# Performance work log

Measured on AMD Instinct MI355X. Metric: run time of the kernel, lower is better.

Reference implementation:

```python
import jax, jax.numpy as jnp
import numpy as np

B, T, D, NH, V, L = 2, 1024, 1024, 16, 32000, 4  # L = blocks * layers_per_block
HD = D // NH
FF = 4 * D


def rmsnorm(x, gamma, beta):
    # matches RMSNorm: mean of squares over last dim (tp pmean is identity on 1 device)
    ms = jnp.mean(jnp.square(x), axis=-1, keepdims=True)
    return (x / jnp.sqrt(ms + 1e-6)) * gamma + beta


def setup_inputs() -> dict:
    key = jax.random.key(0)
    ks = jax.random.split(key, 16)
    s = 0.02
    inp = {
        "tokens": jax.random.randint(ks[0], (B, T), 0, V, dtype=jnp.int32),
        "emb_W": jax.random.normal(ks[1], (V, D), jnp.float32) * s,
        "pos_W": jax.random.normal(ks[2], (T, D), jnp.float32) * s,
        "g1": jnp.ones((L, D), jnp.float32),
        "be1": jnp.zeros((L, D), jnp.float32),
        "Wqkv": jax.random.normal(ks[3], (L, D, 3 * D), jnp.float32) * s,
        "bqkv": jnp.zeros((L, 3 * D), jnp.float32),
        "Wo": jax.random.normal(ks[4], (L, D, D), jnp.float32) * s,
        "bo": jnp.zeros((L, D), jnp.float32),
        "g2": jnp.ones((L, D), jnp.float32),
        "be2": jnp.zeros((L, D), jnp.float32),
        "Wf1": jax.random.normal(ks[5], (L, D, FF), jnp.float32) * s,
        "bf1": jnp.zeros((L, FF), jnp.float32),
        "Wf2": jax.random.normal(ks[6], (L, FF, D), jnp.float32) * s,
        "bf2": jnp.zeros((L, D), jnp.float32),
        "gf": jnp.ones((D,), jnp.float32),
        "bef": jnp.zeros((D,), jnp.float32),
    }
    return inp


def _forward(tokens, emb_W, pos_W, g1, be1, Wqkv, bqkv, Wo, bo, g2, be2,
             Wf1, bf1, Wf2, bf2, gf, bef):
    x = emb_W[tokens] + pos_W[jnp.arange(T)]  # [B, T, D]
    causal = jnp.tril(jnp.ones((T, T), dtype=bool))
    scale = HD ** -0.5
    for i in range(L):
        # attention sub-block
        h = rmsnorm(x, g1[i], be1[i])
        qkv = h @ Wqkv[i] + bqkv[i]
        q, k, v = jnp.split(qkv, 3, axis=-1)
        q = q.reshape(B, T, NH, HD).transpose(0, 2, 1, 3)  # B nh T d
        k = k.reshape(B, T, NH, HD).transpose(0, 2, 1, 3)
        v = v.reshape(B, T, NH, HD).transpose(0, 2, 1, 3)
        att = jnp.einsum('bhqd,bhkd->bhqk', q, k) * scale
        att = jnp.where(causal, att, -jnp.inf)
        att = jax.nn.softmax(att, axis=-1)
        o = jnp.einsum('bhqk,bhkd->bhqd', att, v)
        o = o.transpose(0, 2, 1, 3).reshape(B, T, D)
        x = x + (o @ Wo[i] + bo[i])
        # FFN sub-block (selu, dropout off since train=False)
        h = rmsnorm(x, g2[i], be2[i])
        f = jax.nn.selu(h @ Wf1[i] + bf1[i]) @ Wf2[i] + bf2[i]
        x = x + f
    # tied output head: final RMSNorm then embedding.attend
    x = rmsnorm(x, gf, bef)
    logits = jnp.einsum('btd,vd->btv', x, emb_W)
    return logits


def reference(tokens, emb_W, pos_W, g1, be1, Wqkv, bqkv, Wo, bo, g2, be2,
              Wf1, bf1, Wf2, bf2, gf, bef):
    return _forward(tokens, emb_W, pos_W, g1, be1, Wqkv, bqkv, Wo, bo,
                    g2, be2, Wf1, bf1, Wf2, bf2, gf, bef)
```

## Files before the change

### kernel.cpp

```cpp
#include <hip/hip_runtime.h>

typedef unsigned short u16;
typedef __attribute__((ext_vector_type(8))) short bf16x8;
typedef __attribute__((ext_vector_type(4))) float f32x4;

#define DD 1024
#define TT 1024
#define NHH 16
#define VV 32000
#define FFF 4096
#define LL 4
#define MM 2048
#define TD3 3072

__device__ __forceinline__ u16 f2bfu(float f) {
  unsigned int x = __builtin_bit_cast(unsigned int, f);
  return (u16)((x + 0x7FFFu + ((x >> 16) & 1u)) >> 16);
}

__device__ __forceinline__ void gl16(const u16* g, u16* l) {
  __builtin_amdgcn_global_load_lds((const __attribute__((address_space(1))) void*)g,
                                   (__attribute__((address_space(3))) void*)l, 16, 0, 0);
}

template <int N>
__device__ __forceinline__ void vwait() {
  if constexpr (N == 0) asm volatile("s_waitcnt vmcnt(0)" ::: "memory");
  else asm volatile("s_waitcnt vmcnt(8)" ::: "memory");
}

__global__ void transpose_cvt_k(const float* __restrict__ in, u16* __restrict__ out,
                                int K, int N) {
  const size_t mat = (size_t)K * N;
  in += (size_t)blockIdx.z * mat;
  out += (size_t)blockIdx.z * mat;
  __shared__ float tile[32][33];
  const int n0 = blockIdx.x << 5, k0 = blockIdx.y << 5;
  const int tx = threadIdx.x, ty = threadIdx.y;
#pragma unroll
  for (int i = 0; i < 32; i += 8) tile[ty + i][tx] = in[(size_t)(k0 + ty + i) * N + n0 + tx];
  __syncthreads();
#pragma unroll
  for (int i = 0; i < 32; i += 8)
    out[(size_t)(n0 + ty + i) * K + k0 + tx] = f2bfu(tile[tx][ty + i]);
}

__global__ void cvt_bf16_k(const float* __restrict__ in, u16* __restrict__ out, long n4) {
  const long i = (long)blockIdx.x * blockDim.x + threadIdx.x;
  if (i >= n4) return;
  const float4 v = ((const float4*)in)[i];
  ushort4 o;
  o.x = f2bfu(v.x); o.y = f2bfu(v.y); o.z = f2bfu(v.z); o.w = f2bfu(v.w);
  ((ushort4*)out)[i] = o;
}

__global__ void embed_k(const int* __restrict__ tok, const float* __restrict__ emb,
                        const float* __restrict__ pos, float* __restrict__ x) {
  const int m = blockIdx.x, tid = threadIdx.x;
  const int t = m & (TT - 1);
  const int id = tok[m];
  const float4 e = ((const float4*)(emb + (size_t)id * DD))[tid];
  const float4 p = ((const float4*)(pos + (size_t)t * DD))[tid];
  float4 r;
  r.x = e.x + p.x; r.y = e.y + p.y; r.z = e.z + p.z; r.w = e.w + p.w;
  ((float4*)(x + (size_t)m * DD))[tid] = r;
}

__global__ void rmsnorm_k(const float* __restrict__ x, const float* __restrict__ g,
                          const float* __restrict__ be, u16* __restrict__ out) {
  const int row = blockIdx.x, tid = threadIdx.x;
  const float4 xv = ((const float4*)(x + (size_t)row * DD))[tid];
  float ss = xv.x * xv.x + xv.y * xv.y + xv.z * xv.z + xv.w * xv.w;
#pragma unroll
  for (int o = 32; o; o >>= 1) ss += __shfl_xor(ss, o);
  __shared__ float sm[4];
  if ((tid & 63) == 0) sm[tid >> 6] = ss;
  __syncthreads();
  const float tot = sm[0] + sm[1] + sm[2] + sm[3];
  const float rs = rsqrtf(tot * (1.f / DD) + 1e-6f);
  const float4 gv = ((const float4*)g)[tid];
  const float4 bv = ((const float4*)be)[tid];
  ushort4 o4;
  o4.x = f2bfu(xv.x * rs * gv.x + bv.x);
  o4.y = f2bfu(xv.y * rs * gv.y + bv.y);
  o4.z = f2bfu(xv.z * rs * gv.z + bv.z);
  o4.w = f2bfu(xv.w * rs * gv.w + bv.w);
  ((ushort4*)(out + (size_t)row * DD))[tid] = o4;
}

template <int NP>
__global__ void addres_k(float* __restrict__ x, const float* __restrict__ pp,
                         const float* __restrict__ bias) {
  const int i = blockIdx.x * 256 + threadIdx.x;
  const int col4 = i & (DD / 4 - 1);
  const float4 bv = ((const float4*)bias)[col4];
  float4 s = ((float4*)x)[i];
  s.x += bv.x; s.y += bv.y; s.z += bv.z; s.w += bv.w;
#pragma unroll
  for (int p = 0; p < NP; ++p) {
    const float4 pv = ((const float4*)pp)[(size_t)p * (MM * DD / 4) + i];
    s.x += pv.x; s.y += pv.y; s.z += pv.z; s.w += pv.w;
  }
  ((float4*)x)[i] = s;
}

__global__ void pack_vt_k(const u16* __restrict__ qkv, u16* __restrict__ Vt) {
  const int z = blockIdx.x;
  const int t0 = blockIdx.y << 6;
  const int b = z >> 4, h = z & 15;
  __shared__ u16 tile[64][72];
  const int tid = threadIdx.x;
  for (int c = tid; c < 512; c += 256) {
    const int t = c >> 3, d8 = (c & 7) << 3;
    union { uint4 u; u16 s[8]; } tmp;
    tmp.u = *(const uint4*)(qkv + (long)(b * TT + t0 + t) * TD3 + 2 * DD + h * 64 + d8);
#pragma unroll
    for (int j = 0; j < 8; ++j) tile[d8 + j][t] = tmp.s[j];
  }
  __syncthreads();
  for (int c = tid; c < 512; c += 256) {
    const int d = c >> 3, t8 = (c & 7) << 3;
    *(uint4*)(Vt + ((long)z * 64 + d) * TT + t0 + t8) = *(const uint4*)&tile[d][t8];
  }
}

__global__ __launch_bounds__(256) void flash_k(const u16* __restrict__ qkv,
                                               const u16* __restrict__ Vt,
                                               u16* __restrict__ o) {
  const int z = blockIdx.x;
  const int pair = blockIdx.y;
  const int b = z >> 4, h = z & 15;
  const int tid = threadIdx.x;
  const int lane = tid & 63;
  const int w = tid >> 6;

  __shared__ u16 Qs[64 * 64];
  __shared__ u16 Ks[128 * 64];
  __shared__ u16 Vs[64 * 128];
  __shared__ u16 Ps[64 * 128];

  const u16* qbase = qkv + (size_t)b * TT * TD3;
  const int kcb = (lane >> 4) << 4;

  for (int half = 0; half < 2; ++half) {
    const int qa = half ? (15 - pair) : pair;
    const int q0 = qa << 6;
    const int nkt = (qa >> 1) + 1;

#pragma unroll
    for (int c = 0; c < 2; ++c) {
      const int rbase = c * 32 + w * 8;
      const int row = rbase + (lane >> 3);
      const u16* src = qbase + (long)(q0 + row) * TD3 + h * 64 +
                       ((((lane & 7) << 4) ^ ((row & 7) << 4)) >> 1);
      gl16(src, &Qs[rbase * 64]);
    }

    float m_r[4], l_r[4];
    f32x4 oacc[4];
#pragma unroll
    for (int r = 0; r < 4; ++r) { m_r[r] = -1e30f; l_r[r] = 0.f; }
#pragma unroll
    for (int nd = 0; nd < 4; ++nd) oacc[nd] = (f32x4){0.f, 0.f, 0.f, 0.f};

    for (int kt = 0; kt < nkt; ++kt) {
      const int t0 = kt << 7;
#pragma unroll
      for (int c = 0; c < 4; ++c) {
        const int rbase = c * 32 + w * 8;
        const int row = rbase + (lane >> 3);
        const u16* src = qbase + (long)(t0 + row) * TD3 + DD + h * 64 +
                         ((((lane & 7) << 4) ^ ((row & 7) << 4)) >> 1);
        gl16(src, &Ks[rbase * 64]);
      }
#pragma unroll
      for (int c = 0; c < 4; ++c) {
        const int rbase = c * 16 + w * 4;
        const int d = rbase + (lane >> 4);
        const u16* src = Vt + ((long)(z * 64 + d)) * TT + t0 +
                         ((((lane & 15) << 4) ^ ((d & 7) << 4)) >> 1);
        gl16(src, &Vs[rbase * 128]);
      }
      __syncthreads();

      f32x4 sacc[8];
#pragma unroll
      for (int ni = 0; ni < 8; ++ni) sacc[ni] = (f32x4){0.f, 0.f, 0.f, 0.f};
      const int qrow = (w << 4) + (lane & 15);
#pragma unroll
      for (int ks = 0; ks < 2; ++ks) {
        const bf16x8 aq = *(const bf16x8*)&Qs[qrow * 64 + (((ks * 64 + kcb) ^ ((qrow & 7) << 4)) >> 1)];
#pragma unroll
        for (int ni = 0; ni < 8; ++ni) {
          const int key = (lane & 15) + (ni << 4);
          const bf16x8 bk = *(const bf16x8*)&Ks[key * 64 + (((ks * 64 + kcb) ^ ((key & 7) << 4)) >> 1)];
          sacc[ni] = __builtin_amdgcn_mfma_f32_16x16x32_bf16(aq, bk, sacc[ni], 0, 0, 0);
        }
      }

      float mx[4] = {-1e30f, -1e30f, -1e30f, -1e30f};
      const bool diag = (kt == nkt - 1);
#pragma unroll
      for (int ni = 0; ni < 8; ++ni)
#pragma unroll
        for (int r = 0; r < 4; ++r) {
          float v = sacc[ni][r] * 0.125f;
          if (diag) {
            const int key = t0 + (lane & 15) + (ni << 4);
            const int qq = q0 + (w << 4) + ((lane >> 4) << 2) + r;
            if (key > qq) v = -1e30f;
          }
          sacc[ni][r] = v;
          mx[r] = fmaxf(mx[r], v);
        }
#pragma unroll
      for (int st = 1; st < 16; st <<= 1)
#pragma unroll
        for (int r = 0; r < 4; ++r) mx[r] = fmaxf(mx[r], __shfl_xor(mx[r], st));
      float sc[4], sum[4];
#pragma unroll
      for (int r = 0; r < 4; ++r) {
        const float mn = fmaxf(m_r[r], mx[r]);
        sc[r] = __expf(m_r[r] - mn);
        m_r[r] = mn;
        sum[r] = 0.f;
      }
#pragma unroll
      for (int ni = 0; ni < 8; ++ni)
#pragma unroll
        for (int r = 0; r < 4; ++r) {
          const float e = __expf(sacc[ni][r] - m_r[r]);
          sum[r] += e;
          const int prow = (w << 4) + ((lane >> 4) << 2) + r;
          const int pcol = (lane & 15) + (ni << 4);
          Ps[prow * 128 + (((pcol << 1) ^ ((prow & 7) << 4)) >> 1)] = f2bfu(e);
        }
#pragma unroll
      for (int st = 1; st < 16; st <<= 1)
#pragma unroll
        for (int r = 0; r < 4; ++r) sum[r] += __shfl_xor(sum[r], st);
#pragma unroll
      for (int r = 0; r < 4; ++r) l_r[r] = l_r[r] * sc[r] + sum[r];
#pragma unroll
      for (int nd = 0; nd < 4; ++nd)
#pragma unroll
        for (int r = 0; r < 4; ++r) oacc[nd][r] *= sc[r];

#pragma unroll
      for (int ks2 = 0; ks2 < 4; ++ks2) {
        const int prow = (w << 4) + (lane & 15);
        const bf16x8 pa = *(const bf16x8*)&Ps[prow * 128 + (((ks2 * 64 + kcb) ^ ((prow & 7) << 4)) >> 1)];
#pragma unroll
        for (int nd = 0; nd < 4; ++nd) {
          const int dd2 = (lane & 15) + (nd << 4);
          const bf16x8 vb = *(const bf16x8*)&Vs[dd2 * 128 + (((ks2 * 64 + kcb) ^ ((dd2 & 7) << 4)) >> 1)];
          oacc[nd] = __builtin_amdgcn_mfma_f32_16x16x32_bf16(pa, vb, oacc[nd], 0, 0, 0);
        }
      }
      __syncthreads();
    }

    float inv[4];
#pragma unroll
    for (int r = 0; r < 4; ++r) inv[r] = 1.f / l_r[r];
#pragma unroll
    for (int nd = 0; nd < 4; ++nd)
#pragma unroll
      for (int r = 0; r < 4; ++r) {
        const int row = q0 + (w << 4) + ((lane >> 4) << 2) + r;
        const int col = (h << 6) + (lane & 15) + (nd << 4);
        o[(long)(b * TT + row) * DD + col] = f2bfu(oacc[nd][r] * inv[r]);
      }
  }
}

enum { EPI_BF16 = 0, EPI_BF16_BIAS = 1, EPI_SELU = 2, EPI_F32 = 3, EPI_RESID = 4 };

template <int EPI>
__global__ __launch_bounds__(256) void gemm_bt(
    const u16* __restrict__ A, long az1, long az2, int lda,
    const u16* __restrict__ Bt, long bz1, long bz2, int ldb,
    void* __restrict__ C, long cz1, long cz2, int ldc,
    const float* __restrict__ bias, int Nvalid, int K) {
  const int z = blockIdx.z;
  A += (long)(z >> 4) * az1 + (long)(z & 15) * az2;
  Bt += (long)(z >> 4) * bz1 + (long)(z & 15) * bz2;
  const long coff = (long)(z >> 4) * cz1 + (long)(z & 15) * cz2;

  __shared__ u16 ldsA[2][128 * 32];
  __shared__ u16 ldsB[2][128 * 32];

  const int tid = threadIdx.x;
  const int lane = tid & 63;
  const int wave = tid >> 6;
  const int wr = wave >> 1, wc = wave & 1;
  const int m0 = blockIdx.x << 7, n0 = blockIdx.y << 7;

  f32x4 acc[4][4];
#pragma unroll
  for (int i = 0; i < 4; ++i)
#pragma unroll
    for (int j = 0; j < 4; ++j) acc[i][j] = (f32x4){0.f, 0.f, 0.f, 0.f};

  auto STAGE = [&](int buf, int kt) {
    const int k0 = kt << 5;
#pragma unroll
    for (int p = 0; p < 2; ++p) {
      const int c = tid + (p << 8);
      const int row = c >> 2, col = (c & 3) << 3;
      gl16(A + (long)(m0 + row) * lda + k0 + col, &ldsA[buf][c << 3]);
      gl16(Bt + (long)(n0 + row) * ldb + k0 + col, &ldsB[buf][c << 3]);
    }
  };

  const int nk = K >> 5;
  STAGE(0, 0);
  __syncthreads();
  int cur = 0;
  for (int kt = 0; kt < nk; ++kt) {
    if (kt + 1 < nk) STAGE(cur ^ 1, kt + 1);
    const int rb = lane & 15;
    const int kc = (lane >> 4) << 3;
    bf16x8 af[4], bfr[4];
#pragma unroll
    for (int mi = 0; mi < 4; ++mi)
      af[mi] = *(const bf16x8*)&ldsA[cur][(((wr << 6) + (mi << 4) + rb) << 5) + kc];
#pragma unroll
    for (int ni = 0; ni < 4; ++ni)
      bfr[ni] = *(const bf16x8*)&ldsB[cur][(((wc << 6) + (ni << 4) + rb) << 5) + kc];
#pragma unroll
    for (int mi = 0; mi < 4; ++mi)
#pragma unroll
      for (int ni = 0; ni < 4; ++ni)
        acc[mi][ni] = __builtin_amdgcn_mfma_f32_16x16x32_bf16(af[mi], bfr[ni], acc[mi][ni], 0, 0, 0);
    __syncthreads();
    cur ^= 1;
  }

  const int row0 = m0 + (wr << 6) + ((lane >> 4) << 2);
  const int col0 = n0 + (wc << 6) + (lane & 15);
#pragma unroll
  for (int ni = 0; ni < 4; ++ni) {
    const int col = col0 + (ni << 4);
    if (col >= Nvalid) continue;
    float bv = 0.f;
    if (EPI == EPI_BF16_BIAS || EPI == EPI_SELU || EPI == EPI_RESID) bv = bias[col];
#pragma unroll
    for (int mi = 0; mi < 4; ++mi) {
#pragma unroll
      for (int r = 0; r < 4; ++r) {
        const int row = row0 + (mi << 4) + r;
        const long idx = coff + (long)row * ldc + col;
        float v = acc[mi][ni][r] + bv;
        if (EPI == EPI_SELU)
          v = v > 0.f ? 1.0507009873554805f * v : 1.7580993408473766f * (__expf(v) - 1.f);
        if (EPI == EPI_BF16 || EPI == EPI_BF16_BIAS || EPI == EPI_SELU)
          ((u16*)C)[idx] = f2bfu(v);
        else if (EPI == EPI_F32)
          ((float*)C)[idx] = v;
        else
          ((float*)C)[idx] += v;
      }
    }
  }
}

template <int EPI, int KDIM>
__global__ __launch_bounds__(512) void gemm256_k(
    const u16* __restrict__ A, int lda,
    const u16* __restrict__ Bt, int ldb,
    void* __restrict__ C, int ldc,
    const float* __restrict__ bias, int mm) {
  extern __shared__ u16 smem[];
  u16* SA = smem;
  u16* SB = smem + 32768;

  const int nwg = gridDim.x;
  const int q = nwg >> 3, r = nwg & 7;
  const int xcd = blockIdx.x & 7, loc = blockIdx.x >> 3;
  const int wg = (xcd < r) ? (xcd * (q + 1) + loc) : (r * (q + 1) + (xcd - r) * q + loc);
  const int m0 = (wg % mm) << 8;
  const int n0 = (wg / mm) << 8;

  const int tid = threadIdx.x;
  const int lane = tid & 63;
  const int w = tid >> 6;
  const int wr = w >> 2, wc = w & 3;

  f32x4 acc[8][4];
#pragma unroll
  for (int i = 0; i < 8; ++i)
#pragma unroll
    for (int j = 0; j < 4; ++j) acc[i][j] = (f32x4){0.f, 0.f, 0.f, 0.f};

  auto STAGE = [&](int p, int kt) {
    u16* la = SA + (p << 14);
    u16* lb = SB + (p << 14);
    const int k0 = kt << 6;
#pragma unroll
    for (int hh = 0; hh < 4; ++hh) {
      const int c = tid + (hh << 9);
      const int row = c >> 3, slot = c & 7;
      const int col = k0 + ((slot ^ (row & 7)) << 3);
      gl16(A + (size_t)(m0 + row) * lda + col, la + (c << 3));
      gl16(Bt + (size_t)(n0 + row) * ldb + col, lb + (c << 3));
    }
  };

  constexpr int NK = KDIM >> 6;
  STAGE(0, 0);
  STAGE(1, 1);

#pragma unroll 1
  for (int t = 0; t < NK; ++t) {
    if (t + 1 < NK) vwait<8>();
    else vwait<0>();
    __builtin_amdgcn_s_barrier();
    __builtin_amdgcn_sched_barrier(0);

    const u16* a = SA + ((t & 1) << 14);
    const u16* b = SB + ((t & 1) << 14);
    bf16x8 af[8][2], bfr[4][2];
#pragma unroll
    for (int ks = 0; ks < 2; ++ks) {
#pragma unroll
      for (int mi = 0; mi < 8; ++mi) {
        const int row = (wr << 7) + (mi << 4) + (lane & 15);
        const int slot = ((ks << 2) + (lane >> 4)) ^ (row & 7);
        af[mi][ks] = *(const bf16x8*)&a[(row << 6) + (slot << 3)];
      }
#pragma unroll
      for (int ni = 0; ni < 4; ++ni) {
        const int row = (wc << 6) + (ni << 4) + (lane & 15);
        const int slot = ((ks << 2) + (lane >> 4)) ^ (row & 7);
        bfr[ni][ks] = *(const bf16x8*)&b[(row << 6) + (slot << 3)];
      }
    }
    asm volatile("s_waitcnt lgkmcnt(0)" ::: "memory");
    __builtin_amdgcn_sched_barrier(0);
    __builtin_amdgcn_s_barrier();
    __builtin_amdgcn_sched_barrier(0);
    if (t + 2 < NK) STAGE(t & 1, t + 2);

    __builtin_amdgcn_s_setprio(1);
#pragma unroll
    for (int ks = 0; ks < 2; ++ks)
#pragma unroll
      for (int mi = 0; mi < 8; ++mi)
#pragma unroll
        for (int ni = 0; ni < 4; ++ni)
          acc[mi][ni] = __builtin_amdgcn_mfma_f32_16x16x32_bf16(af[mi][ks], bfr[ni][ks], acc[mi][ni], 0, 0, 0);
    __builtin_amdgcn_s_setprio(0);
  }

  const int row0 = m0 + (wr << 7) + ((lane >> 4) << 2);
  const int col0 = n0 + (wc << 6) + (lane & 15);
#pragma unroll
  for (int ni = 0; ni < 4; ++ni) {
    const int col = col0 + (ni << 4);
    float bv = 0.f;
    if (EPI == EPI_BF16_BIAS || EPI == EPI_SELU) bv = bias[col];
#pragma unroll
    for (int mi = 0; mi < 8; ++mi) {
#pragma unroll
      for (int r = 0; r < 4; ++r) {
        const int row = row0 + (mi << 4) + r;
        const long idx = (long)row * ldc + col;
        float v = acc[mi][ni][r] + bv;
        if (EPI == EPI_SELU)
          v = v > 0.f ? 1.0507009873554805f * v : 1.7580993408473766f * (__expf(v) - 1.f);
        if (EPI == EPI_BF16 || EPI == EPI_BF16_BIAS || EPI == EPI_SELU)
          ((u16*)C)[idx] = f2bfu(v);
        else
          ((float*)C)[idx] = v;
      }
    }
  }
}

extern "C" void kernel_launch(void* const* d_in, const int* in_sizes, int n_in,
                              void* d_out, int out_size, void* d_ws, size_t ws_size,
                              hipStream_t stream) {
  const int* tokens = (const int*)d_in[0];
  const float* emb_W = (const float*)d_in[1];
  const float* pos_W = (const float*)d_in[2];
  const float* g1 = (const float*)d_in[3];
  const float* be1 = (const float*)d_in[4];
  const float* Wqkv = (const float*)d_in[5];
  const float* bqkv = (const float*)d_in[6];
  const float* Wo = (const float*)d_in[7];
  const float* bo = (const float*)d_in[8];
  const float* g2 = (const float*)d_in[9];
  const float* be2 = (const float*)d_in[10];
  const float* Wf1 = (const float*)d_in[11];
  const float* bf1 = (const float*)d_in[12];
  const float* Wf2 = (const float*)d_in[13];
  const float* bf2 = (const float*)d_in[14];
  const float* gf = (const float*)d_in[15];
  const float* bef = (const float*)d_in[16];

  char* w = (char*)d_ws;
  auto alloc = [&](size_t bytes) {
    char* p = w;
    w += (bytes + 255) & ~(size_t)255;
    return p;
  };
  u16* WqkvT = (u16*)alloc((size_t)LL * TD3 * DD * 2);
  u16* WoT   = (u16*)alloc((size_t)LL * DD * DD * 2);
  u16* Wf1T  = (u16*)alloc((size_t)LL * FFF * DD * 2);
  u16* Wf2T  = (u16*)alloc((size_t)LL * DD * FFF * 2);
  u16* embB  = (u16*)alloc((size_t)VV * DD * 2);
  float* x   = (float*)alloc((size_t)MM * DD * 4);
  u16* h     = (u16*)alloc((size_t)MM * DD * 2);
  u16* qkv   = (u16*)alloc((size_t)MM * TD3 * 2);
  u16* Vt    = (u16*)alloc((size_t)32 * 64 * TT * 2);
  u16* o     = (u16*)alloc((size_t)MM * DD * 2);
  u16* h1    = (u16*)alloc((size_t)MM * FFF * 2);
  u16* xn    = (u16*)alloc((size_t)MM * DD * 2);
  float* pp  = (float*)alloc((size_t)4 * MM * DD * 4);

  bool big =
      hipFuncSetAttribute((const void*)&gemm256_k<EPI_F32, 1024>,
                          hipFuncAttributeMaxDynamicSharedMemorySize, 131072) == hipSuccess;

  dim3 tb(32, 8);
  transpose_cvt_k<<<dim3(TD3 / 32, DD / 32, LL), tb, 0, stream>>>(Wqkv, WqkvT, DD, TD3);
  transpose_cvt_k<<<dim3(DD / 32, DD / 32, LL), tb, 0, stream>>>(Wo, WoT, DD, DD);
  transpose_cvt_k<<<dim3(FFF / 32, DD / 32, LL), tb, 0, stream>>>(Wf1, Wf1T, DD, FFF);
  transpose_cvt_k<<<dim3(DD / 32, FFF / 32, LL), tb, 0, stream>>>(Wf2, Wf2T, FFF, DD);
  cvt_bf16_k<<<(VV * DD / 4) / 256, 256, 0, stream>>>(emb_W, embB, (long)VV * DD / 4);
  embed_k<<<MM, 256, 0, stream>>>(tokens, emb_W, pos_W, x);

  for (int i = 0; i < LL; ++i) {
    rmsnorm_k<<<MM, 256, 0, stream>>>(x, g1 + i * DD, be1 + i * DD, h);
    gemm_bt<EPI_BF16_BIAS><<<dim3(16, 24, 1), 256, 0, stream>>>(
        h, 0, 0, DD, WqkvT + (size_t)i * TD3 * DD, 0, 0, DD,
        qkv, 0, 0, TD3, bqkv + i * TD3, TD3, DD);
    pack_vt_k<<<dim3(32, 16), 256, 0, stream>>>(qkv, Vt);
    flash_k<<<dim3(32, 8), 256, 0, stream>>>(qkv, Vt, o);
    gemm_bt<EPI_F32><<<dim3(16, 8, 2), 256, 0, stream>>>(
        o, 0, 512, DD, WoT + (size_t)i * DD * DD, 0, 512, DD,
        pp, 0, (long)MM * DD, DD, nullptr, DD, 512);
    addres_k<2><<<MM * DD / 4 / 256, 256, 0, stream>>>(x, pp, bo + i * DD);
    rmsnorm_k<<<MM, 256, 0, stream>>>(x, g2 + i * DD, be2 + i * DD, h);
    gemm_bt<EPI_SELU><<<dim3(16, 32, 1), 256, 0, stream>>>(
        h, 0, 0, DD, Wf1T + (size_t)i * FFF * DD, 0, 0, DD,
        h1, 0, 0, FFF, bf1 + i * FFF, FFF, DD);
    gemm_bt<EPI_F32><<<dim3(16, 8, 4), 256, 0, stream>>>(
        h1, 0, 1024, FFF, Wf2T + (size_t)i * DD * FFF, 0, 1024, FFF,
        pp, 0, (long)MM * DD, DD, nullptr, DD, 1024);
    addres_k<4><<<MM * DD / 4 / 256, 256, 0, stream>>>(x, pp, bf2 + i * DD);
  }

  rmsnorm_k<<<MM, 256, 0, stream>>>(x, gf, bef, xn);
  if (big) {
    gemm256_k<EPI_F32, 1024><<<1000, 512, 131072, stream>>>(
        xn, DD, embB, DD, (float*)d_out, VV, nullptr, 8);
  } else {
    gemm_bt<EPI_F32><<<dim3(16, 250, 1), 256, 0, stream>>>(
        xn, 0, 0, DD, embB, 0, 0, DD,
        (float*)d_out, 0, 0, VV, nullptr, VV, DD);
  }
}
```

Before: 1.008 ms.

## Fuse residual add with RMSNorm and triple-buffer the LM-head GEMM

Residual-add kernels now also compute the following RMSNorm (next layer's pre-attention norm, or the final norm), which drops separate rmsnorm launches and a re-read of x. The large vocabulary GEMM switches from a two-stage, K=64 pipeline to a three-stage, K=32 pipeline with a new LDS layout. It interleaves LDS fragment reads with MFMA groups, aiming to hide load latency and use less shared memory (96KB instead of 128KB). The cost is more barriers per K and more complex swizzle indexing.

```diff
diff --git a/kernel.cpp b/kernel.cpp
--- a/kernel.cpp
+++ b/kernel.cpp
@@ -26,6 +26,7 @@
 template <int N>
 __device__ __forceinline__ void vwait() {
   if constexpr (N == 0) asm volatile("s_waitcnt vmcnt(0)" ::: "memory");
+  else if constexpr (N == 4) asm volatile("s_waitcnt vmcnt(4)" ::: "memory");
   else asm volatile("s_waitcnt vmcnt(8)" ::: "memory");
 }
 
@@ -89,19 +90,36 @@
 }
 
 template <int NP>
-__global__ void addres_k(float* __restrict__ x, const float* __restrict__ pp,
-                         const float* __restrict__ bias) {
-  const int i = blockIdx.x * 256 + threadIdx.x;
-  const int col4 = i & (DD / 4 - 1);
-  const float4 bv = ((const float4*)bias)[col4];
-  float4 s = ((float4*)x)[i];
+__global__ void addres_rms_k(float* __restrict__ x, const float* __restrict__ pp,
+                             const float* __restrict__ bias, const float* __restrict__ g,
+                             const float* __restrict__ be, u16* __restrict__ out) {
+  const int row = blockIdx.x, tid = threadIdx.x;
+  const size_t base = (size_t)row * (DD / 4) + tid;
+  float4 s = ((float4*)x)[base];
+  const float4 bv = ((const float4*)bias)[tid];
   s.x += bv.x; s.y += bv.y; s.z += bv.z; s.w += bv.w;
 #pragma unroll
   for (int p = 0; p < NP; ++p) {
-    const float4 pv = ((const float4*)pp)[(size_t)p * (MM * DD / 4) + i];
+    const float4 pv = ((const float4*)pp)[(size_t)p * (MM * DD / 4) + base];
     s.x += pv.x; s.y += pv.y; s.z += pv.z; s.w += pv.w;
   }
-  ((float4*)x)[i] = s;
+  ((float4*)x)[base] = s;
+  float ss = s.x * s.x + s.y * s.y + s.z * s.z + s.w * s.w;
+#pragma unroll
+  for (int o = 32; o; o >>= 1) ss += __shfl_xor(ss, o);
+  __shared__ float sm[4];
+  if ((tid & 63) == 0) sm[tid >> 6] = ss;
+  __syncthreads();
+  const float tot = sm[0] + sm[1] + sm[2] + sm[3];
+  const float rs = rsqrtf(tot * (1.f / DD) + 1e-6f);
+  const float4 gv = ((const float4*)g)[tid];
+  const float4 bev = ((const float4*)be)[tid];
+  ushort4 o4;
+  o4.x = f2bfu(s.x * rs * gv.x + bev.x);
+  o4.y = f2bfu(s.y * rs * gv.y + bev.y);
+  o4.z = f2bfu(s.z * rs * gv.z + bev.z);
+  o4.w = f2bfu(s.w * rs * gv.w + bev.w);
+  ((ushort4*)(out + (size_t)row * DD))[tid] = o4;
 }
 
 __global__ void pack_vt_k(const u16* __restrict__ qkv, u16* __restrict__ Vt) {
@@ -373,7 +391,7 @@
     const float* __restrict__ bias, int mm) {
   extern __shared__ u16 smem[];
   u16* SA = smem;
-  u16* SB = smem + 32768;
+  u16* SB = smem + 24576;
 
   const int nwg = gridDim.x;
   const int q = nwg >> 3, r = nwg & 7;
@@ -386,6 +404,7 @@
   const int lane = tid & 63;
   const int w = tid >> 6;
   const int wr = w >> 2, wc = w & 3;
+  const int l = lane & 15, kq = lane >> 4;
 
   f32x4 acc[8][4];
 #pragma unroll
@@ -394,63 +413,101 @@
     for (int j = 0; j < 4; ++j) acc[i][j] = (f32x4){0.f, 0.f, 0.f, 0.f};
 
   auto STAGE = [&](int p, int kt) {
-    u16* la = SA + (p << 14);
-    u16* lb = SB + (p << 14);
-    const int k0 = kt << 6;
-#pragma unroll
-    for (int hh = 0; hh < 4; ++hh) {
+    u16* la = SA + (p << 13);
+    u16* lb = SB + (p << 13);
+    const int k0 = kt << 5;
+#pragma unroll
+    for (int hh = 0; hh < 2; ++hh) {
       const int c = tid + (hh << 9);
-      const int row = c >> 3, slot = c & 7;
-      const int col = k0 + ((slot ^ (row & 7)) << 3);
+      const int r2 = c >> 3, sp = c & 7;
+      const int s = sp ^ (r2 & 7);
+      const int row = r2 + ((s >> 2) << 7);
+      const int col = k0 + ((s & 3) << 3);
       gl16(A + (size_t)(m0 + row) * lda + col, la + (c << 3));
       gl16(Bt + (size_t)(n0 + row) * ldb + col, lb + (c << 3));
     }
   };
 
-  constexpr int NK = KDIM >> 6;
+  constexpr int NK = KDIM >> 5;
   STAGE(0, 0);
   STAGE(1, 1);
-
+  STAGE(2, 2);
+
+  int buf = 0;
 #pragma unroll 1
   for (int t = 0; t < NK; ++t) {
-    if (t + 1 < NK) vwait<8>();
+    if (t + 2 < NK) vwait<8>();
+    else if (t + 1 < NK) vwait<4>();
     else vwait<0>();
     __builtin_amdgcn_s_barrier();
     __builtin_amdgcn_sched_barrier(0);
 
-    const u16* a = SA + ((t & 1) << 14);
-    const u16* b = SB + ((t & 1) << 14);
-    bf16x8 af[8][2], bfr[4][2];
-#pragma unroll
-    for (int ks = 0; ks < 2; ++ks) {
-#pragma unroll
-      for (int mi = 0; mi < 8; ++mi) {
-        const int row = (wr << 7) + (mi << 4) + (lane & 15);
-        const int slot = ((ks << 2) + (lane >> 4)) ^ (row & 7);
-        af[mi][ks] = *(const bf16x8*)&a[(row << 6) + (slot << 3)];
-      }
-#pragma unroll
-      for (int ni = 0; ni < 4; ++ni) {
-        const int row = (wc << 6) + (ni << 4) + (lane & 15);
-        const int slot = ((ks << 2) + (lane >> 4)) ^ (row & 7);
-        bfr[ni][ks] = *(const bf16x8*)&b[(row << 6) + (slot << 3)];
-      }
-    }
+    const u16* a = SA + (buf << 13);
+    const u16* b = SB + (buf << 13);
+    auto rdA = [&](int mi) -> bf16x8 {
+      const int row = (wr << 7) + (mi << 4) + l;
+      const int r2 = row & 127;
+      const int sp = (((row >> 7) << 2) + kq) ^ (r2 & 7);
+      return *(const bf16x8*)&a[(r2 << 6) + (sp << 3)];
+    };
+    auto rdB = [&](int ni) -> bf16x8 {
+      const int row = (wc << 6) + (ni << 4) + l;
+      const int r2 = row & 127;
+      const int sp = (((row >> 7) << 2) + kq) ^ (r2 & 7);
+      return *(const bf16x8*)&b[(r2 << 6) + (sp << 3)];
+    };
+
+    bf16x8 bfr[4], afA[2], afB[2];
+    bfr[0] = rdB(0); bfr[1] = rdB(1); bfr[2] = rdB(2); bfr[3] = rdB(3);
+    afA[0] = rdA(0); afA[1] = rdA(1);
+    __builtin_amdgcn_sched_barrier(0);
+    afB[0] = rdA(2); afB[1] = rdA(3);
+    __builtin_amdgcn_sched_barrier(0);
+
+    __builtin_amdgcn_s_setprio(1);
+#pragma unroll
+    for (int ni = 0; ni < 4; ++ni) {
+      acc[0][ni] = __builtin_amdgcn_mfma_f32_16x16x32_bf16(afA[0], bfr[ni], acc[0][ni], 0, 0, 0);
+      acc[1][ni] = __builtin_amdgcn_mfma_f32_16x16x32_bf16(afA[1], bfr[ni], acc[1][ni], 0, 0, 0);
+    }
+    __builtin_amdgcn_s_setprio(0);
+    __builtin_amdgcn_sched_barrier(0);
+    afA[0] = rdA(4); afA[1] = rdA(5);
+    __builtin_amdgcn_sched_barrier(0);
+    __builtin_amdgcn_s_setprio(1);
+#pragma unroll
+    for (int ni = 0; ni < 4; ++ni) {
+      acc[2][ni] = __builtin_amdgcn_mfma_f32_16x16x32_bf16(afB[0], bfr[ni], acc[2][ni], 0, 0, 0);
+      acc[3][ni] = __builtin_amdgcn_mfma_f32_16x16x32_bf16(afB[1], bfr[ni], acc[3][ni], 0, 0, 0);
+    }
+    __builtin_amdgcn_s_setprio(0);
+    __builtin_amdgcn_sched_barrier(0);
+    afB[0] = rdA(6); afB[1] = rdA(7);
+    __builtin_amdgcn_sched_barrier(0);
+    __builtin_amdgcn_s_setprio(1);
+#pragma unroll
+    for (int ni = 0; ni < 4; ++ni) {
+      acc[4][ni] = __builtin_amdgcn_mfma_f32_16x16x32_bf16(afA[0], bfr[ni], acc[4][ni], 0, 0, 0);
+      acc[5][ni] = __builtin_amdgcn_mfma_f32_16x16x32_bf16(afA[1], bfr[ni], acc[5][ni], 0, 0, 0);
+    }
+    __builtin_amdgcn_s_setprio(0);
+    __builtin_amdgcn_sched_barrier(0);
+
     asm volatile("s_waitcnt lgkmcnt(0)" ::: "memory");
     __builtin_amdgcn_sched_barrier(0);
     __builtin_amdgcn_s_barrier();
     __builtin_amdgcn_sched_barrier(0);
-    if (t + 2 < NK) STAGE(t & 1, t + 2);
+    if (t + 3 < NK) STAGE(buf, t + 3);
+    __builtin_amdgcn_sched_barrier(0);
 
     __builtin_amdgcn_s_setprio(1);
 #pragma unroll
-    for (int ks = 0; ks < 2; ++ks)
-#pragma unroll
-      for (int mi = 0; mi < 8; ++mi)
-#pragma unroll
-        for (int ni = 0; ni < 4; ++ni)
-          acc[mi][ni] = __builtin_amdgcn_mfma_f32_16x16x32_bf16(af[mi][ks], bfr[ni][ks], acc[mi][ni], 0, 0, 0);
+    for (int ni = 0; ni < 4; ++ni) {
+      acc[6][ni] = __builtin_amdgcn_mfma_f32_16x16x32_bf16(afB[0], bfr[ni], acc[6][ni], 0, 0, 0);
+      acc[7][ni] = __builtin_amdgcn_mfma_f32_16x16x32_bf16(afB[1], bfr[ni], acc[7][ni], 0, 0, 0);
+    }
     __builtin_amdgcn_s_setprio(0);
+    buf = (buf == 2) ? 0 : buf + 1;
   }
 
   const int row0 = m0 + (wr << 7) + ((lane >> 4) << 2);
@@ -516,12 +573,11 @@
   u16* Vt    = (u16*)alloc((size_t)32 * 64 * TT * 2);
   u16* o     = (u16*)alloc((size_t)MM * DD * 2);
   u16* h1    = (u16*)alloc((size_t)MM * FFF * 2);
-  u16* xn    = (u16*)alloc((size_t)MM * DD * 2);
   float* pp  = (float*)alloc((size_t)4 * MM * DD * 4);
 
   bool big =
       hipFuncSetAttribute((const void*)&gemm256_k<EPI_F32, 1024>,
-                          hipFuncAttributeMaxDynamicSharedMemorySize, 131072) == hipSuccess;
+                          hipFuncAttributeMaxDynamicSharedMemorySize, 98304) == hipSuccess;
 
   dim3 tb(32, 8);
   transpose_cvt_k<<<dim3(TD3 / 32, DD / 32, LL), tb, 0, stream>>>(Wqkv, WqkvT, DD, TD3);
@@ -530,9 +586,9 @@
   transpose_cvt_k<<<dim3(DD / 32, FFF / 32, LL), tb, 0, stream>>>(Wf2, Wf2T, FFF, DD);
   cvt_bf16_k<<<(VV * DD / 4) / 256, 256, 0, stream>>>(emb_W, embB, (long)VV * DD / 4);
   embed_k<<<MM, 256, 0, stream>>>(tokens, emb_W, pos_W, x);
+  rmsnorm_k<<<MM, 256, 0, stream>>>(x, g1, be1, h);
 
   for (int i = 0; i < LL; ++i) {
-    rmsnorm_k<<<MM, 256, 0, stream>>>(x, g1 + i * DD, be1 + i * DD, h);
     gemm_bt<EPI_BF16_BIAS><<<dim3(16, 24, 1), 256, 0, stream>>>(
         h, 0, 0, DD, WqkvT + (size_t)i * TD3 * DD, 0, 0, DD,
         qkv, 0, 0, TD3, bqkv + i * TD3, TD3, DD);
@@ -541,24 +597,25 @@
     gemm_bt<EPI_F32><<<dim3(16, 8, 2), 256, 0, stream>>>(
         o, 0, 512, DD, WoT + (size_t)i * DD * DD, 0, 512, DD,
         pp, 0, (long)MM * DD, DD, nullptr, DD, 512);
-    addres_k<2><<<MM * DD / 4 / 256, 256, 0, stream>>>(x, pp, bo + i * DD);
-    rmsnorm_k<<<MM, 256, 0, stream>>>(x, g2 + i * DD, be2 + i * DD, h);
+    addres_rms_k<2><<<MM, 256, 0, stream>>>(x, pp, bo + i * DD, g2 + i * DD, be2 + i * DD, h);
     gemm_bt<EPI_SELU><<<dim3(16, 32, 1), 256, 0, stream>>>(
         h, 0, 0, DD, Wf1T + (size_t)i * FFF * DD, 0, 0, DD,
         h1, 0, 0, FFF, bf1 + i * FFF, FFF, DD);
     gemm_bt<EPI_F32><<<dim3(16, 8, 4), 256, 0, stream>>>(
         h1, 0, 1024, FFF, Wf2T + (size_t)i * DD * FFF, 0, 1024, FFF,
         pp, 0, (long)MM * DD, DD, nullptr, DD, 1024);
-    addres_k<4><<<MM * DD / 4 / 256, 256, 0, stream>>>(x, pp, bf2 + i * DD);
-  }
-
-  rmsnorm_k<<<MM, 256, 0, stream>>>(x, gf, bef, xn);
+    const bool last = (i == LL - 1);
+    addres_rms_k<4><<<MM, 256, 0, stream>>>(
+        x, pp, bf2 + i * DD,
+        last ? gf : g1 + (i + 1) * DD, last ? bef : be1 + (i + 1) * DD, h);
+  }
+
   if (big) {
-    gemm256_k<EPI_F32, 1024><<<1000, 512, 131072, stream>>>(
-        xn, DD, embB, DD, (float*)d_out, VV, nullptr, 8);
+    gemm256_k<EPI_F32, 1024><<<1000, 512, 98304, stream>>>(
+        h, DD, embB, DD, (float*)d_out, VV, nullptr, 8);
   } else {
     gemm_bt<EPI_F32><<<dim3(16, 250, 1), 256, 0, stream>>>(
-        xn, 0, 0, DD, embB, 0, 0, DD,
+        h, 0, 0, DD, embB, 0, 0, DD,
         (float*)d_out, 0, 0, VV, nullptr, VV, DD);
   }
 }
```

Result: no change. 993.8 us (-1.4%).
